# Kernel tuning notes

Hardware: AMD Instinct MI355X
Metric: run time of the kernel (lower is better)

Reference implementation:

```python
import jax, jax.numpy as jnp
import numpy as np

N_NODES, N_EDGES, N_INC = 50000, 10000, 800000
IN_C, HID_C, OUT_C = 128, 128, 128
EPS = 1e-5  # BatchNorm1d default


def setup_inputs() -> dict:
    key = jax.random.key(0)
    ks = jax.random.split(key, 6)
    x = jax.random.normal(ks[0], (N_NODES, IN_C), jnp.float32)
    node_idx = jax.random.randint(ks[1], (N_INC,), 0, N_NODES)
    edge_idx = jax.random.randint(ks[2], (N_INC,), 0, N_EDGES)
    hyperedge_index = jnp.stack([node_idx, edge_idx])  # [2, nnz]
    hyperedge_weight = jnp.ones((N_EDGES,), jnp.float32)
    s1 = 1.0 / np.sqrt(IN_C)
    s2 = 1.0 / np.sqrt(HID_C)
    W1 = jax.random.uniform(ks[3], (HID_C, IN_C), jnp.float32, -s1, s1)
    b1 = jnp.zeros((HID_C,), jnp.float32)
    gamma = jnp.ones((HID_C,), jnp.float32)
    beta = jnp.zeros((HID_C,), jnp.float32)
    W2 = jax.random.uniform(ks[4], (OUT_C, HID_C), jnp.float32, -s2, s2)
    b2 = jnp.zeros((OUT_C,), jnp.float32)
    return dict(x=x, hyperedge_index=hyperedge_index, hyperedge_weight=hyperedge_weight,
                W1=W1, b1=b1, gamma=gamma, beta=beta, W2=W2, b2=b2)


def _hconv(x, W, b, node_idx, edge_idx, hw):
    """PyG HypergraphConv (heads=1, no attention): D^-1 H B^-1 H^T (X W^T) + b."""
    x = x @ W.T  # [N, out_c]; lin has bias=False in PyG
    # node degrees weighted by hyperedge weight
    D = jax.ops.segment_sum(hw[edge_idx], node_idx, num_segments=N_NODES)
    Dinv = jnp.where(D > 0, 1.0 / D, 0.0)
    # hyperedge degrees
    Bdeg = jax.ops.segment_sum(jnp.ones_like(edge_idx, dtype=x.dtype), edge_idx,
                               num_segments=N_EDGES)
    Binv = jnp.where(Bdeg > 0, 1.0 / Bdeg, 0.0)
    # node -> hyperedge: e_e = B_e^-1 * sum_{i in e} x_i
    e = jax.ops.segment_sum(Binv[edge_idx][:, None] * x[node_idx], edge_idx,
                            num_segments=N_EDGES)
    # hyperedge -> node: out_i = D_i^-1 * sum_{e ni i} e_e
    out = jax.ops.segment_sum(Dinv[node_idx][:, None] * e[edge_idx], node_idx,
                              num_segments=N_NODES)
    return out + b  # PyG adds bias after propagation


def reference(x, hyperedge_index, hyperedge_weight, W1, b1, gamma, beta, W2, b2):
    node_idx, edge_idx = hyperedge_index[0], hyperedge_index[1]
    h = _hconv(x, W1, b1, node_idx, edge_idx, hyperedge_weight)
    # BatchNorm1d (training mode: batch statistics, biased variance)
    mu = h.mean(axis=0)
    var = h.var(axis=0)
    h = gamma * (h - mu) * jax.lax.rsqrt(var + EPS) + beta
    return _hconv(h, W2, b2, node_idx, edge_idx, hyperedge_weight)
```

## Files before the change

kernel.cpp:

```cpp
#include <hip/hip_runtime.h>

#define NN 50000
#define NE 10000
#define NI 800000
#define CH 128
#define EPSV 1e-5f
#define ESTR 160
#define NSTR 64

__global__ __launch_bounds__(256) void k_fill_ell(const int* __restrict__ nidx,
    const int* __restrict__ eidx, int* __restrict__ cnt_e,
    int* __restrict__ cnt_n, int* __restrict__ ell_e, int* __restrict__ ell_n) {
  int i = blockIdx.x * 256 + threadIdx.x;
  if (i >= NI) return;
  int n = nidx[i], e = eidx[i];
  int ce = atomicAdd(&cnt_e[e], 1);
  if (ce < ESTR) ell_e[e * ESTR + ce] = n;
  int cn = atomicAdd(&cnt_n[n], 1);
  if (cn < NSTR) ell_n[n * NSTR + cn] = e;
}

__global__ __launch_bounds__(256) void k_gather_edge(const int* __restrict__ cnt_e,
    const int* __restrict__ ell_e, const float* __restrict__ X,
    float* __restrict__ M) {
  int gid = blockIdx.x * 256 + threadIdx.x;
  int e = gid >> 5;
  if (e >= NE) return;
  int c = (gid & 31) * 4;
  int t = cnt_e[e];
  if (t > ESTR) t = ESTR;
  const int* base = &ell_e[e * ESTR];
  float4 acc = make_float4(0.f, 0.f, 0.f, 0.f);
  int j = 0;
  for (; j + 4 <= t; j += 4) {
    int4 nn = *reinterpret_cast<const int4*>(base + j);
    float4 v0 = *reinterpret_cast<const float4*>(&X[(long)nn.x * CH + c]);
    float4 v1 = *reinterpret_cast<const float4*>(&X[(long)nn.y * CH + c]);
    float4 v2 = *reinterpret_cast<const float4*>(&X[(long)nn.z * CH + c]);
    float4 v3 = *reinterpret_cast<const float4*>(&X[(long)nn.w * CH + c]);
    acc.x += (v0.x + v1.x) + (v2.x + v3.x);
    acc.y += (v0.y + v1.y) + (v2.y + v3.y);
    acc.z += (v0.z + v1.z) + (v2.z + v3.z);
    acc.w += (v0.w + v1.w) + (v2.w + v3.w);
  }
  for (; j < t; ++j) {
    int n = base[j];
    float4 v = *reinterpret_cast<const float4*>(&X[(long)n * CH + c]);
    acc.x += v.x; acc.y += v.y; acc.z += v.z; acc.w += v.w;
  }
  float binv = (t > 0) ? 1.f / (float)t : 0.f;
  float4 o = make_float4(acc.x * binv, acc.y * binv, acc.z * binv, acc.w * binv);
  *reinterpret_cast<float4*>(&M[(long)e * CH + c]) = o;
}

__global__ __launch_bounds__(256) void k_gather_node(const int* __restrict__ cnt_n,
    const int* __restrict__ ell_n, const float* __restrict__ hw,
    const float* __restrict__ Eacc, const float* __restrict__ bias,
    float* __restrict__ Out) {
  int gid = blockIdx.x * 256 + threadIdx.x;
  int i = gid >> 5;
  if (i >= NN) return;
  int c = (gid & 31) * 4;
  const float4 bb = *reinterpret_cast<const float4*>(&bias[c]);
  int t = cnt_n[i];
  if (t > NSTR) t = NSTR;
  const int* base = &ell_n[i * NSTR];
  float4 acc = make_float4(0.f, 0.f, 0.f, 0.f);
  float wsum = 0.f;
  int j = 0;
  for (; j + 4 <= t; j += 4) {
    int4 ee = *reinterpret_cast<const int4*>(base + j);
    wsum += (hw[ee.x] + hw[ee.y]) + (hw[ee.z] + hw[ee.w]);
    float4 v0 = *reinterpret_cast<const float4*>(&Eacc[(long)ee.x * CH + c]);
    float4 v1 = *reinterpret_cast<const float4*>(&Eacc[(long)ee.y * CH + c]);
    float4 v2 = *reinterpret_cast<const float4*>(&Eacc[(long)ee.z * CH + c]);
    float4 v3 = *reinterpret_cast<const float4*>(&Eacc[(long)ee.w * CH + c]);
    acc.x += (v0.x + v1.x) + (v2.x + v3.x);
    acc.y += (v0.y + v1.y) + (v2.y + v3.y);
    acc.z += (v0.z + v1.z) + (v2.z + v3.z);
    acc.w += (v0.w + v1.w) + (v2.w + v3.w);
  }
  for (; j < t; ++j) {
    int e = base[j];
    wsum += hw[e];
    float4 v = *reinterpret_cast<const float4*>(&Eacc[(long)e * CH + c]);
    acc.x += v.x; acc.y += v.y; acc.z += v.z; acc.w += v.w;
  }
  float dinv = wsum > 0.f ? 1.f / wsum : 0.f;
  float4 o;
  o.x = dinv * acc.x + bb.x; o.y = dinv * acc.y + bb.y;
  o.z = dinv * acc.z + bb.z; o.w = dinv * acc.w + bb.w;
  *reinterpret_cast<float4*>(&Out[(long)i * CH + c]) = o;
}

__global__ __launch_bounds__(256) void k_colstats(const float* __restrict__ H,
    float* __restrict__ colsum, float* __restrict__ colsq) {
  const int tid = threadIdx.x;
  const int cp = (tid & 63) * 2;
  const int rh = tid >> 6;
  float s0 = 0, s1 = 0, q0 = 0, q1 = 0;
  for (int r = blockIdx.x * 4 + rh; r < NN; r += gridDim.x * 4) {
    float2 v = *reinterpret_cast<const float2*>(&H[(long)r * CH + cp]);
    s0 += v.x; s1 += v.y; q0 += v.x * v.x; q1 += v.y * v.y;
  }
  __shared__ float sh[256][4];
  sh[tid][0] = s0; sh[tid][1] = s1; sh[tid][2] = q0; sh[tid][3] = q1;
  __syncthreads();
  if (tid < 64) {
    float ts0 = 0, ts1 = 0, tq0 = 0, tq1 = 0;
    #pragma unroll
    for (int g = 0; g < 4; ++g) {
      ts0 += sh[tid + g * 64][0]; ts1 += sh[tid + g * 64][1];
      tq0 += sh[tid + g * 64][2]; tq1 += sh[tid + g * 64][3];
    }
    atomicAdd(&colsum[cp], ts0); atomicAdd(&colsum[cp + 1], ts1);
    atomicAdd(&colsq[cp], tq0);  atomicAdd(&colsq[cp + 1], tq1);
  }
}

__global__ void k_bn_params(const float* __restrict__ colsum,
    const float* __restrict__ colsq, const float* __restrict__ gamma,
    const float* __restrict__ beta, float* __restrict__ scl,
    float* __restrict__ shf) {
  int c = threadIdx.x;
  if (c >= CH) return;
  float mu = colsum[c] * (1.f / NN);
  float var = colsq[c] * (1.f / NN) - mu * mu;
  float a = gamma[c] * rsqrtf(var + EPSV);
  scl[c] = a;
  shf[c] = beta[c] - mu * a;
}

__global__ __launch_bounds__(256) void k_gemm(const float* __restrict__ A,
    const float* __restrict__ W, float* __restrict__ Out, int nrows,
    const float* __restrict__ scale, const float* __restrict__ shift) {
  __shared__ float As[32][132];
  const int tid = threadIdx.x;
  const int row0 = blockIdx.x * 32;

  #pragma unroll
  for (int rep = 0; rep < 4; ++rep) {
    int idx = rep * 256 + tid;
    int r = idx >> 5, kq = idx & 31;
    int gr = row0 + r;
    float4 v = make_float4(0.f, 0.f, 0.f, 0.f);
    if (gr < nrows) v = *reinterpret_cast<const float4*>(&A[(long)gr * CH + kq * 4]);
    if (scale) {
      v.x = scale[kq * 4 + 0] * v.x + shift[kq * 4 + 0];
      v.y = scale[kq * 4 + 1] * v.y + shift[kq * 4 + 1];
      v.z = scale[kq * 4 + 2] * v.z + shift[kq * 4 + 2];
      v.w = scale[kq * 4 + 3] * v.w + shift[kq * 4 + 3];
    }
    As[r][kq * 4 + 0] = v.x; As[r][kq * 4 + 1] = v.y;
    As[r][kq * 4 + 2] = v.z; As[r][kq * 4 + 3] = v.w;
  }
  __syncthreads();

  const int tx = tid & 31, ty = tid >> 5;
  const int r0 = ty * 4, c0 = tx * 4;
  float acc[4][4];
  #pragma unroll
  for (int i = 0; i < 4; ++i)
    #pragma unroll
    for (int j = 0; j < 4; ++j) acc[i][j] = 0.f;

  #pragma unroll 4
  for (int kq = 0; kq < 32; ++kq) {
    float4 a0 = *reinterpret_cast<const float4*>(&As[r0 + 0][kq * 4]);
    float4 a1 = *reinterpret_cast<const float4*>(&As[r0 + 1][kq * 4]);
    float4 a2 = *reinterpret_cast<const float4*>(&As[r0 + 2][kq * 4]);
    float4 a3 = *reinterpret_cast<const float4*>(&As[r0 + 3][kq * 4]);
    float4 w0 = *reinterpret_cast<const float4*>(&W[(long)(c0 + 0) * CH + kq * 4]);
    float4 w1 = *reinterpret_cast<const float4*>(&W[(long)(c0 + 1) * CH + kq * 4]);
    float4 w2 = *reinterpret_cast<const float4*>(&W[(long)(c0 + 2) * CH + kq * 4]);
    float4 w3 = *reinterpret_cast<const float4*>(&W[(long)(c0 + 3) * CH + kq * 4]);
    const float4 aa[4] = {a0, a1, a2, a3};
    const float4 ww[4] = {w0, w1, w2, w3};
    #pragma unroll
    for (int i = 0; i < 4; ++i)
      #pragma unroll
      for (int j = 0; j < 4; ++j)
        acc[i][j] += aa[i].x * ww[j].x + aa[i].y * ww[j].y +
                     aa[i].z * ww[j].z + aa[i].w * ww[j].w;
  }

  #pragma unroll
  for (int i = 0; i < 4; ++i) {
    int gr = row0 + r0 + i;
    if (gr < nrows) {
      float4 o = make_float4(acc[i][0], acc[i][1], acc[i][2], acc[i][3]);
      *reinterpret_cast<float4*>(&Out[(long)gr * CH + c0]) = o;
    }
  }
}

extern "C" void kernel_launch(void* const* d_in, const int* in_sizes, int n_in,
                              void* d_out, int out_size, void* d_ws, size_t ws_size,
                              hipStream_t stream) {
  const float* x     = (const float*)d_in[0];
  const int*   hidx  = (const int*)d_in[1];
  const float* hw    = (const float*)d_in[2];
  const float* W1    = (const float*)d_in[3];
  const float* b1    = (const float*)d_in[4];
  const float* gamma = (const float*)d_in[5];
  const float* beta  = (const float*)d_in[6];
  const float* W2    = (const float*)d_in[7];
  const float* b2    = (const float*)d_in[8];
  float* out = (float*)d_out;

  const int* nidx = hidx;
  const int* eidx = hidx + NI;

  int* wi = (int*)d_ws;
  int* cnt_e = wi;
  int* cnt_n = cnt_e + NE;
  int* ell_e = cnt_n + NN;
  int* ell_n = ell_e + (long)NE * ESTR;
  long int_elems = (long)NE + NN + (long)NE * ESTR + (long)NN * NSTR;
  int_elems = (int_elems + 3) & ~3L;
  float* wf = (float*)d_ws + int_elems;
  float* colsum = wf;
  float* colsq  = wf + 128;
  float* scl    = wf + 256;
  float* shf    = wf + 384;
  float* M      = wf + 512;
  float* Eacc   = M + (long)NE * CH;
  float* H      = out;

  hipMemsetAsync(cnt_e, 0, (size_t)(NE + NN) * sizeof(int), stream);
  hipMemsetAsync(colsum, 0, 256 * sizeof(float), stream);
  k_fill_ell<<<(NI + 255) / 256, 256, 0, stream>>>(nidx, eidx, cnt_e, cnt_n,
                                                   ell_e, ell_n);

  k_gather_edge<<<(NE * 32 + 255) / 256, 256, 0, stream>>>(cnt_e, ell_e, x, M);
  k_gemm<<<(NE + 31) / 32, 256, 0, stream>>>(M, W1, Eacc, NE, nullptr, nullptr);
  k_gather_node<<<(NN * 32 + 255) / 256, 256, 0, stream>>>(cnt_n, ell_n, hw,
                                                           Eacc, b1, H);
  k_colstats<<<512, 256, 0, stream>>>(H, colsum, colsq);
  k_bn_params<<<1, 128, 0, stream>>>(colsum, colsq, gamma, beta, scl, shf);

  k_gather_edge<<<(NE * 32 + 255) / 256, 256, 0, stream>>>(cnt_e, ell_e, H, M);
  k_gemm<<<(NE + 31) / 32, 256, 0, stream>>>(M, W2, Eacc, NE, scl, shf);
  k_gather_node<<<(NN * 32 + 255) / 256, 256, 0, stream>>>(cnt_n, ell_n, hw,
                                                           Eacc, b2, out);
}
```

Before: 482.4 us.

## Fuse hyperedge gather into GEMM and store ELL indices as 16-bit

Result: no change. 490.9 us (+1.8%).

```diff
diff --git a/kernel.cpp b/kernel.cpp
--- a/kernel.cpp
+++ b/kernel.cpp
@@ -10,154 +10,65 @@
 
 __global__ __launch_bounds__(256) void k_fill_ell(const int* __restrict__ nidx,
     const int* __restrict__ eidx, int* __restrict__ cnt_e,
-    int* __restrict__ cnt_n, int* __restrict__ ell_e, int* __restrict__ ell_n) {
+    int* __restrict__ cnt_n, unsigned short* __restrict__ ell_e,
+    unsigned short* __restrict__ ell_n) {
   int i = blockIdx.x * 256 + threadIdx.x;
   if (i >= NI) return;
   int n = nidx[i], e = eidx[i];
   int ce = atomicAdd(&cnt_e[e], 1);
-  if (ce < ESTR) ell_e[e * ESTR + ce] = n;
+  if (ce < ESTR) ell_e[(long)e * ESTR + ce] = (unsigned short)n;
   int cn = atomicAdd(&cnt_n[n], 1);
-  if (cn < NSTR) ell_n[n * NSTR + cn] = e;
-}
-
-__global__ __launch_bounds__(256) void k_gather_edge(const int* __restrict__ cnt_e,
-    const int* __restrict__ ell_e, const float* __restrict__ X,
-    float* __restrict__ M) {
-  int gid = blockIdx.x * 256 + threadIdx.x;
-  int e = gid >> 5;
-  if (e >= NE) return;
-  int c = (gid & 31) * 4;
-  int t = cnt_e[e];
-  if (t > ESTR) t = ESTR;
-  const int* base = &ell_e[e * ESTR];
-  float4 acc = make_float4(0.f, 0.f, 0.f, 0.f);
-  int j = 0;
-  for (; j + 4 <= t; j += 4) {
-    int4 nn = *reinterpret_cast<const int4*>(base + j);
-    float4 v0 = *reinterpret_cast<const float4*>(&X[(long)nn.x * CH + c]);
-    float4 v1 = *reinterpret_cast<const float4*>(&X[(long)nn.y * CH + c]);
-    float4 v2 = *reinterpret_cast<const float4*>(&X[(long)nn.z * CH + c]);
-    float4 v3 = *reinterpret_cast<const float4*>(&X[(long)nn.w * CH + c]);
-    acc.x += (v0.x + v1.x) + (v2.x + v3.x);
-    acc.y += (v0.y + v1.y) + (v2.y + v3.y);
-    acc.z += (v0.z + v1.z) + (v2.z + v3.z);
-    acc.w += (v0.w + v1.w) + (v2.w + v3.w);
-  }
-  for (; j < t; ++j) {
-    int n = base[j];
-    float4 v = *reinterpret_cast<const float4*>(&X[(long)n * CH + c]);
-    acc.x += v.x; acc.y += v.y; acc.z += v.z; acc.w += v.w;
-  }
-  float binv = (t > 0) ? 1.f / (float)t : 0.f;
-  float4 o = make_float4(acc.x * binv, acc.y * binv, acc.z * binv, acc.w * binv);
-  *reinterpret_cast<float4*>(&M[(long)e * CH + c]) = o;
-}
-
-__global__ __launch_bounds__(256) void k_gather_node(const int* __restrict__ cnt_n,
-    const int* __restrict__ ell_n, const float* __restrict__ hw,
-    const float* __restrict__ Eacc, const float* __restrict__ bias,
-    float* __restrict__ Out) {
-  int gid = blockIdx.x * 256 + threadIdx.x;
-  int i = gid >> 5;
-  if (i >= NN) return;
-  int c = (gid & 31) * 4;
-  const float4 bb = *reinterpret_cast<const float4*>(&bias[c]);
-  int t = cnt_n[i];
-  if (t > NSTR) t = NSTR;
-  const int* base = &ell_n[i * NSTR];
-  float4 acc = make_float4(0.f, 0.f, 0.f, 0.f);
-  float wsum = 0.f;
-  int j = 0;
-  for (; j + 4 <= t; j += 4) {
-    int4 ee = *reinterpret_cast<const int4*>(base + j);
-    wsum += (hw[ee.x] + hw[ee.y]) + (hw[ee.z] + hw[ee.w]);
-    float4 v0 = *reinterpret_cast<const float4*>(&Eacc[(long)ee.x * CH + c]);
-    float4 v1 = *reinterpret_cast<const float4*>(&Eacc[(long)ee.y * CH + c]);
-    float4 v2 = *reinterpret_cast<const float4*>(&Eacc[(long)ee.z * CH + c]);
-    float4 v3 = *reinterpret_cast<const float4*>(&Eacc[(long)ee.w * CH + c]);
-    acc.x += (v0.x + v1.x) + (v2.x + v3.x);
-    acc.y += (v0.y + v1.y) + (v2.y + v3.y);
-    acc.z += (v0.z + v1.z) + (v2.z + v3.z);
-    acc.w += (v0.w + v1.w) + (v2.w + v3.w);
-  }
-  for (; j < t; ++j) {
-    int e = base[j];
-    wsum += hw[e];
-    float4 v = *reinterpret_cast<const float4*>(&Eacc[(long)e * CH + c]);
-    acc.x += v.x; acc.y += v.y; acc.z += v.z; acc.w += v.w;
-  }
-  float dinv = wsum > 0.f ? 1.f / wsum : 0.f;
-  float4 o;
-  o.x = dinv * acc.x + bb.x; o.y = dinv * acc.y + bb.y;
-  o.z = dinv * acc.z + bb.z; o.w = dinv * acc.w + bb.w;
-  *reinterpret_cast<float4*>(&Out[(long)i * CH + c]) = o;
-}
-
-__global__ __launch_bounds__(256) void k_colstats(const float* __restrict__ H,
-    float* __restrict__ colsum, float* __restrict__ colsq) {
-  const int tid = threadIdx.x;
-  const int cp = (tid & 63) * 2;
-  const int rh = tid >> 6;
-  float s0 = 0, s1 = 0, q0 = 0, q1 = 0;
-  for (int r = blockIdx.x * 4 + rh; r < NN; r += gridDim.x * 4) {
-    float2 v = *reinterpret_cast<const float2*>(&H[(long)r * CH + cp]);
-    s0 += v.x; s1 += v.y; q0 += v.x * v.x; q1 += v.y * v.y;
-  }
-  __shared__ float sh[256][4];
-  sh[tid][0] = s0; sh[tid][1] = s1; sh[tid][2] = q0; sh[tid][3] = q1;
-  __syncthreads();
-  if (tid < 64) {
-    float ts0 = 0, ts1 = 0, tq0 = 0, tq1 = 0;
-    #pragma unroll
-    for (int g = 0; g < 4; ++g) {
-      ts0 += sh[tid + g * 64][0]; ts1 += sh[tid + g * 64][1];
-      tq0 += sh[tid + g * 64][2]; tq1 += sh[tid + g * 64][3];
-    }
-    atomicAdd(&colsum[cp], ts0); atomicAdd(&colsum[cp + 1], ts1);
-    atomicAdd(&colsq[cp], tq0);  atomicAdd(&colsq[cp + 1], tq1);
-  }
-}
-
-__global__ void k_bn_params(const float* __restrict__ colsum,
-    const float* __restrict__ colsq, const float* __restrict__ gamma,
-    const float* __restrict__ beta, float* __restrict__ scl,
-    float* __restrict__ shf) {
-  int c = threadIdx.x;
-  if (c >= CH) return;
-  float mu = colsum[c] * (1.f / NN);
-  float var = colsq[c] * (1.f / NN) - mu * mu;
-  float a = gamma[c] * rsqrtf(var + EPSV);
-  scl[c] = a;
-  shf[c] = beta[c] - mu * a;
-}
-
-__global__ __launch_bounds__(256) void k_gemm(const float* __restrict__ A,
-    const float* __restrict__ W, float* __restrict__ Out, int nrows,
+  if (cn < NSTR) ell_n[(long)n * NSTR + cn] = (unsigned short)e;
+}
+
+__global__ __launch_bounds__(256) void k_edge_gemm(const int* __restrict__ cnt_e,
+    const unsigned short* __restrict__ ell_e, const float* __restrict__ X,
+    const float* __restrict__ W, float* __restrict__ Eout,
     const float* __restrict__ scale, const float* __restrict__ shift) {
   __shared__ float As[32][132];
   const int tid = threadIdx.x;
-  const int row0 = blockIdx.x * 32;
-
-  #pragma unroll
-  for (int rep = 0; rep < 4; ++rep) {
-    int idx = rep * 256 + tid;
-    int r = idx >> 5, kq = idx & 31;
-    int gr = row0 + r;
-    float4 v = make_float4(0.f, 0.f, 0.f, 0.f);
-    if (gr < nrows) v = *reinterpret_cast<const float4*>(&A[(long)gr * CH + kq * 4]);
+  const int e0 = blockIdx.x * 32;
+  const int lane = tid & 31, grp = tid >> 5;
+  const int c = lane * 4;
+
+  for (int it = 0; it < 4; ++it) {
+    int r = it * 8 + grp;
+    int e = e0 + r;
+    int t = 0;
+    if (e < NE) { t = cnt_e[e]; if (t > ESTR) t = ESTR; }
+    const unsigned short* base = ell_e + (long)e * ESTR;
+    float4 acc = make_float4(0.f, 0.f, 0.f, 0.f);
+    int j = 0;
+    for (; j + 4 <= t; j += 4) {
+      ushort4 nn = *reinterpret_cast<const ushort4*>(base + j);
+      float4 v0 = *reinterpret_cast<const float4*>(&X[(long)nn.x * CH + c]);
+      float4 v1 = *reinterpret_cast<const float4*>(&X[(long)nn.y * CH + c]);
+      float4 v2 = *reinterpret_cast<const float4*>(&X[(long)nn.z * CH + c]);
+      float4 v3 = *reinterpret_cast<const float4*>(&X[(long)nn.w * CH + c]);
+      acc.x += (v0.x + v1.x) + (v2.x + v3.x);
+      acc.y += (v0.y + v1.y) + (v2.y + v3.y);
+      acc.z += (v0.z + v1.z) + (v2.z + v3.z);
+      acc.w += (v0.w + v1.w) + (v2.w + v3.w);
+    }
+    for (; j < t; ++j) {
+      int n = base[j];
+      float4 v = *reinterpret_cast<const float4*>(&X[(long)n * CH + c]);
+      acc.x += v.x; acc.y += v.y; acc.z += v.z; acc.w += v.w;
+    }
+    float binv = (t > 0) ? 1.f / (float)t : 0.f;
+    float4 m = make_float4(acc.x * binv, acc.y * binv, acc.z * binv, acc.w * binv);
     if (scale) {
-      v.x = scale[kq * 4 + 0] * v.x + shift[kq * 4 + 0];
-      v.y = scale[kq * 4 + 1] * v.y + shift[kq * 4 + 1];
-      v.z = scale[kq * 4 + 2] * v.z + shift[kq * 4 + 2];
-      v.w = scale[kq * 4 + 3] * v.w + shift[kq * 4 + 3];
-    }
-    As[r][kq * 4 + 0] = v.x; As[r][kq * 4 + 1] = v.y;
-    As[r][kq * 4 + 2] = v.z; As[r][kq * 4 + 3] = v.w;
+      m.x = scale[c + 0] * m.x + shift[c + 0];
+      m.y = scale[c + 1] * m.y + shift[c + 1];
+      m.z = scale[c + 2] * m.z + shift[c + 2];
+      m.w = scale[c + 3] * m.w + shift[c + 3];
+    }
+    As[r][c + 0] = m.x; As[r][c + 1] = m.y;
+    As[r][c + 2] = m.z; As[r][c + 3] = m.w;
   }
   __syncthreads();
 
-  const int tx = tid & 31, ty = tid >> 5;
-  const int r0 = ty * 4, c0 = tx * 4;
+  const int r0 = grp * 4, c0 = lane * 4;
   float acc[4][4];
   #pragma unroll
   for (int i = 0; i < 4; ++i)
@@ -186,12 +97,90 @@
 
   #pragma unroll
   for (int i = 0; i < 4; ++i) {
-    int gr = row0 + r0 + i;
-    if (gr < nrows) {
+    int ge = e0 + r0 + i;
+    if (ge < NE) {
       float4 o = make_float4(acc[i][0], acc[i][1], acc[i][2], acc[i][3]);
-      *reinterpret_cast<float4*>(&Out[(long)gr * CH + c0]) = o;
-    }
-  }
+      *reinterpret_cast<float4*>(&Eout[(long)ge * CH + c0]) = o;
+    }
+  }
+}
+
+__global__ __launch_bounds__(256) void k_gather_node(const int* __restrict__ cnt_n,
+    const unsigned short* __restrict__ ell_n, const float* __restrict__ hw,
+    const float* __restrict__ Eacc, const float* __restrict__ bias,
+    float* __restrict__ Out) {
+  int gid = blockIdx.x * 256 + threadIdx.x;
+  int i = gid >> 5;
+  if (i >= NN) return;
+  int c = (gid & 31) * 4;
+  const float4 bb = *reinterpret_cast<const float4*>(&bias[c]);
+  int t = cnt_n[i];
+  if (t > NSTR) t = NSTR;
+  const unsigned short* base = ell_n + (long)i * NSTR;
+  float4 acc = make_float4(0.f, 0.f, 0.f, 0.f);
+  float wsum = 0.f;
+  int j = 0;
+  for (; j + 4 <= t; j += 4) {
+    ushort4 ee = *reinterpret_cast<const ushort4*>(base + j);
+    wsum += (hw[ee.x] + hw[ee.y]) + (hw[ee.z] + hw[ee.w]);
+    float4 v0 = *reinterpret_cast<const float4*>(&Eacc[(long)ee.x * CH + c]);
+    float4 v1 = *reinterpret_cast<const float4*>(&Eacc[(long)ee.y * CH + c]);
+    float4 v2 = *reinterpret_cast<const float4*>(&Eacc[(long)ee.z * CH + c]);
+    float4 v3 = *reinterpret_cast<const float4*>(&Eacc[(long)ee.w * CH + c]);
+    acc.x += (v0.x + v1.x) + (v2.x + v3.x);
+    acc.y += (v0.y + v1.y) + (v2.y + v3.y);
+    acc.z += (v0.z + v1.z) + (v2.z + v3.z);
+    acc.w += (v0.w + v1.w) + (v2.w + v3.w);
+  }
+  for (; j < t; ++j) {
+    int e = base[j];
+    wsum += hw[e];
+    float4 v = *reinterpret_cast<const float4*>(&Eacc[(long)e * CH + c]);
+    acc.x += v.x; acc.y += v.y; acc.z += v.z; acc.w += v.w;
+  }
+  float dinv = wsum > 0.f ? 1.f / wsum : 0.f;
+  float4 o;
+  o.x = dinv * acc.x + bb.x; o.y = dinv * acc.y + bb.y;
+  o.z = dinv * acc.z + bb.z; o.w = dinv * acc.w + bb.w;
+  *reinterpret_cast<float4*>(&Out[(long)i * CH + c]) = o;
+}
+
+__global__ __launch_bounds__(256) void k_colstats(const float* __restrict__ H,
+    float* __restrict__ colsum, float* __restrict__ colsq) {
+  const int tid = threadIdx.x;
+  const int cp = (tid & 63) * 2;
+  const int rh = tid >> 6;
+  float s0 = 0, s1 = 0, q0 = 0, q1 = 0;
+  for (int r = blockIdx.x * 4 + rh; r < NN; r += gridDim.x * 4) {
+    float2 v = *reinterpret_cast<const float2*>(&H[(long)r * CH + cp]);
+    s0 += v.x; s1 += v.y; q0 += v.x * v.x; q1 += v.y * v.y;
+  }
+  __shared__ float sh[256][4];
+  sh[tid][0] = s0; sh[tid][1] = s1; sh[tid][2] = q0; sh[tid][3] = q1;
+  __syncthreads();
+  if (tid < 64) {
+    float ts0 = 0, ts1 = 0, tq0 = 0, tq1 = 0;
+    #pragma unroll
+    for (int g = 0; g < 4; ++g) {
+      ts0 += sh[tid + g * 64][0]; ts1 += sh[tid + g * 64][1];
+      tq0 += sh[tid + g * 64][2]; tq1 += sh[tid + g * 64][3];
+    }
+    atomicAdd(&colsum[cp], ts0); atomicAdd(&colsum[cp + 1], ts1);
+    atomicAdd(&colsq[cp], tq0);  atomicAdd(&colsq[cp + 1], tq1);
+  }
+}
+
+__global__ void k_bn_params(const float* __restrict__ colsum,
+    const float* __restrict__ colsq, const float* __restrict__ gamma,
+    const float* __restrict__ beta, float* __restrict__ scl,
+    float* __restrict__ shf) {
+  int c = threadIdx.x;
+  if (c >= CH) return;
+  float mu = colsum[c] * (1.f / NN);
+  float var = colsq[c] * (1.f / NN) - mu * mu;
+  float a = gamma[c] * rsqrtf(var + EPSV);
+  scl[c] = a;
+  shf[c] = beta[c] - mu * a;
 }
 
 extern "C" void kernel_launch(void* const* d_in, const int* in_sizes, int n_in,
@@ -211,20 +200,19 @@
   const int* nidx = hidx;
   const int* eidx = hidx + NI;
 
-  int* wi = (int*)d_ws;
-  int* cnt_e = wi;
+  char* wb = (char*)d_ws;
+  int* cnt_e = (int*)wb;
   int* cnt_n = cnt_e + NE;
-  int* ell_e = cnt_n + NN;
-  int* ell_n = ell_e + (long)NE * ESTR;
-  long int_elems = (long)NE + NN + (long)NE * ESTR + (long)NN * NSTR;
-  int_elems = (int_elems + 3) & ~3L;
-  float* wf = (float*)d_ws + int_elems;
+  unsigned short* ell_e = (unsigned short*)(cnt_n + NN);
+  unsigned short* ell_n = ell_e + (long)NE * ESTR;
+  size_t bytes = (size_t)(NE + NN) * 4 + ((size_t)NE * ESTR + (size_t)NN * NSTR) * 2;
+  bytes = (bytes + 15) & ~(size_t)15;
+  float* wf = (float*)(wb + bytes);
   float* colsum = wf;
   float* colsq  = wf + 128;
   float* scl    = wf + 256;
   float* shf    = wf + 384;
-  float* M      = wf + 512;
-  float* Eacc   = M + (long)NE * CH;
+  float* Eacc   = wf + 512;
   float* H      = out;
 
   hipMemsetAsync(cnt_e, 0, (size_t)(NE + NN) * sizeof(int), stream);
@@ -232,15 +220,15 @@
   k_fill_ell<<<(NI + 255) / 256, 256, 0, stream>>>(nidx, eidx, cnt_e, cnt_n,
                                                    ell_e, ell_n);
 
-  k_gather_edge<<<(NE * 32 + 255) / 256, 256, 0, stream>>>(cnt_e, ell_e, x, M);
-  k_gemm<<<(NE + 31) / 32, 256, 0, stream>>>(M, W1, Eacc, NE, nullptr, nullptr);
+  k_edge_gemm<<<(NE + 31) / 32, 256, 0, stream>>>(cnt_e, ell_e, x, W1, Eacc,
+                                                  nullptr, nullptr);
   k_gather_node<<<(NN * 32 + 255) / 256, 256, 0, stream>>>(cnt_n, ell_n, hw,
                                                            Eacc, b1, H);
   k_colstats<<<512, 256, 0, stream>>>(H, colsum, colsq);
   k_bn_params<<<1, 128, 0, stream>>>(colsum, colsq, gamma, beta, scl, shf);
 
-  k_gather_edge<<<(NE * 32 + 255) / 256, 256, 0, stream>>>(cnt_e, ell_e, H, M);
-  k_gemm<<<(NE + 31) / 32, 256, 0, stream>>>(M, W2, Eacc, NE, scl, shf);
+  k_edge_gemm<<<(NE + 31) / 32, 256, 0, stream>>>(cnt_e, ell_e, H, W2, Eacc,
+                                                  scl, shf);
   k_gather_node<<<(NN * 32 + 255) / 256, 256, 0, stream>>>(cnt_n, ell_n, hw,
                                                            Eacc, b2, out);
 }
```
